# Kernel optimization log

Hardware: AMD Instinct MI355X
Metric: run time of the kernel (lower is better)

Reference implementation:

```python
import jax, jax.numpy as jnp
import numpy as np

B, S, DM, H, NM, PRED = 32, 512, 512, 8, 4, 96
DK = DM // H
C1 = (NM + 7) // 2  # 5
C2 = (NM + 7) // 4  # 2
FC_IN = C2 * (S // 2)  # 512
EPS_NORM = 1e-12
EPS_LN = 1e-5


def _pos_encoding(seq_len, d):
    pos = np.arange(seq_len, dtype=np.float32)[:, None]
    div = np.exp(np.arange(0, d, 2, dtype=np.float32) * (-np.log(10000.0) / d))
    pe = np.zeros((seq_len, d), np.float32)
    pe[:, 0::2] = np.sin(pos * div)
    pe[:, 1::2] = np.cos(pos * div)
    return jnp.asarray(pe)

PE = _pos_encoding(S, DM)


def setup_inputs() -> dict:
    key = jax.random.key(0)
    ks = jax.random.split(key, 24)
    g = lambda k, shape, s: (jax.random.normal(k, shape, dtype=jnp.float32) * s)
    inp = {
        "x": g(ks[0], (B, S, 7), 1.0),
        "emb_W": g(ks[1], (4, DM), 0.5),
        "emb_b": jnp.zeros((DM,), jnp.float32),
        "Wq": g(ks[2], (NM, DM, DM), DM ** -0.5),
        "bq": jnp.zeros((NM, DM), jnp.float32),
        "Wk": g(ks[3], (NM, DM, DM), DM ** -0.5),
        "bk": jnp.zeros((NM, DM), jnp.float32),
        "Wv": g(ks[4], (NM, DM, DM), DM ** -0.5),
        "bv": jnp.zeros((NM, DM), jnp.float32),
        "Wo": g(ks[5], (NM, DM, DM), DM ** -0.5),
        "bo": jnp.zeros((NM, DM), jnp.float32),
        "conv1_w": g(ks[6], (C1, NM * DM, 3), (NM * DM * 3) ** -0.5),
        "conv1_b": jnp.zeros((C1,), jnp.float32),
        "conv2_w": g(ks[7], (C2, C1, 3), (C1 * 3) ** -0.5),
        "conv2_b": jnp.zeros((C2,), jnp.float32),
        "fc1_w": g(ks[8], (FC_IN, 256), FC_IN ** -0.5),
        "fc1_b": jnp.zeros((256,), jnp.float32),
        "fc2_w": g(ks[9], (256, 128), 256 ** -0.5),
        "fc2_b": jnp.zeros((128,), jnp.float32),
        "fc3_w": g(ks[10], (128, PRED), 128 ** -0.5),
        "fc3_b": jnp.zeros((PRED,), jnp.float32),
        "ln_g": jnp.ones((PRED,), jnp.float32),
        "ln_b": jnp.zeros((PRED,), jnp.float32),
    }
    return inp


def _l2norm(v):
    n = jnp.linalg.norm(v, axis=-1, keepdims=True)
    return v / jnp.maximum(n, EPS_NORM)


def reference(x, emb_W, emb_b, Wq, bq, Wk, bk, Wv, bv, Wo, bo,
              conv1_w, conv1_b, conv2_w, conv2_b,
              fc1_w, fc1_b, fc2_w, fc2_b, fc3_w, fc3_b, ln_g, ln_b):
    b, s, _ = x.shape
    static = x[:, :, :3]                     # [B,S,3]
    dynamic = x[:, :, 3:]                    # [B,S,4]
    # per-modality input: [dynamic_i | static] -> [B,M,S,4]
    mod_in = jnp.concatenate([
        dynamic.transpose(0, 2, 1)[..., None],
        jnp.broadcast_to(static[:, None], (b, NM, s, 3)),
    ], axis=-1)
    h = jnp.einsum('bmsf,fd->bmsd', mod_in, emb_W) + emb_b  # shared embedding
    h = h + PE[None, None, :s, :]

    # per-modality multi-head cosine attention (stacked over modality axis m)
    def proj(W, bias):
        y = jnp.einsum('bmsd,mde->bmse', h, W) + bias[None, :, None, :]
        return y.reshape(b, NM, s, H, DK).transpose(0, 1, 3, 2, 4)  # [B,M,H,S,DK]

    Q = _l2norm(proj(Wq, bq))
    K = _l2norm(proj(Wk, bk))
    V = proj(Wv, bv)
    scores = jnp.einsum('bmhsk,bmhtk->bmhst', Q, K)
    attn = jax.nn.softmax(scores, axis=-1)
    ctx = jnp.einsum('bmhst,bmhtk->bmhsk', attn, V)
    ctx = ctx.transpose(0, 1, 3, 2, 4).reshape(b, NM, s, DM)
    out = jnp.einsum('bmsd,mde->bmse', ctx, Wo) + bo[None, :, None, :]

    # concat modalities along feature dim: [B,S,M*DM]
    combined = out.transpose(0, 2, 1, 3).reshape(b, s, NM * DM)

    # conv stack (NCW layout), kernel 3, padding 1
    c = combined.transpose(0, 2, 1)  # [B, M*DM, S]
    dn = ('NCH', 'OIH', 'NCH')
    c = jax.lax.conv_general_dilated(c, conv1_w, (1,), ((1, 1),), dimension_numbers=dn) + conv1_b[None, :, None]
    c = jax.nn.elu(c)
    c = jax.lax.conv_general_dilated(c, conv2_w, (1,), ((1, 1),), dimension_numbers=dn) + conv2_b[None, :, None]
    c = jax.nn.elu(c)
    # max pool k=2 stride=2
    c = c.reshape(b, C2, s // 2, 2).max(axis=-1)
    flat = c.reshape(b, -1)  # [B, FC_IN]

    z = jax.nn.elu(flat @ fc1_w + fc1_b)
    z = jax.nn.elu(z @ fc2_w + fc2_b)
    z = z @ fc3_w + fc3_b  # [B, PRED]

    mu = jnp.mean(z, axis=-1, keepdims=True)
    var = jnp.var(z, axis=-1, keepdims=True)
    z = (z - mu) / jnp.sqrt(var + EPS_LN) * ln_g + ln_b
    return z.reshape(b, PRED, 1)
```

## Files before the change

### kernel.cpp

```cpp
#include <hip/hip_runtime.h>
#include <math.h>

typedef unsigned short u16;
typedef unsigned int u32;
typedef __attribute__((ext_vector_type(8))) short short8;
typedef __attribute__((ext_vector_type(4))) float f32x4;
typedef __attribute__((ext_vector_type(16))) float f32x16;
typedef __attribute__((ext_vector_type(4))) u32 u32x4;
typedef __attribute__((ext_vector_type(2))) u32 u32x2;

__device__ inline u16 f2b(float f) {
  u32 u = __builtin_bit_cast(u32, f);
  u32 r = u + 0x7fffu + ((u >> 16) & 1u);
  return (u16)(r >> 16);
}
__device__ inline float b2f(u16 b) {
  return __builtin_bit_cast(float, (u32)b << 16);
}
__device__ inline u32 cvtpk(float lo, float hi) {
  u32 r;
  asm("v_cvt_pk_bf16_f32 %0, %1, %2" : "=v"(r) : "v"(lo), "v"(hi));
  return r;
}
__device__ inline float eluf(float x) { return x > 0.f ? x : expf(x) - 1.f; }

__device__ inline f32x4 mfma16(short8 a, short8 b, f32x4 c) {
  return __builtin_amdgcn_mfma_f32_16x16x32_bf16(a, b, c, 0, 0, 0);
}
__device__ inline f32x16 mfma32(short8 a, short8 b, f32x16 c) {
  return __builtin_amdgcn_mfma_f32_32x32x16_bf16(a, b, c, 0, 0, 0);
}
__device__ inline void gload16(const u16* g, u16* l) {
  __builtin_amdgcn_global_load_lds((__attribute__((address_space(1))) void*)(g),
                                   (__attribute__((address_space(3))) void*)(l),
                                   16, 0, 0);
}

__global__ __launch_bounds__(256) void prep_misc(
    const float* __restrict__ emb_b, const float* __restrict__ bq,
    const float* __restrict__ bk, const float* __restrict__ bv,
    const float* __restrict__ Wq, const float* __restrict__ Wk,
    const float* __restrict__ Wv, const float* __restrict__ embW,
    const float* __restrict__ Wo, const float* __restrict__ bo,
    const float* __restrict__ w1, u16* __restrict__ A_pe,
    float* __restrict__ pb_bias, float* __restrict__ EW,
    u16* __restrict__ WEFFT, float* __restrict__ bias_t,
    u16* __restrict__ WTqkv) {
  __shared__ float smem[64 * 65];
  const int bid = blockIdx.x, t = threadIdx.x;
  if (bid < 512) {
    int s = bid;
    float div = expf((2.f * t) * (-9.210340371976184f / 512.f));
    float arg = (float)s * div;
    A_pe[s * 512 + 2 * t] = f2b(sinf(arg) + emb_b[2 * t]);
    A_pe[s * 512 + 2 * t + 1] = f2b(cosf(arg) + emb_b[2 * t + 1]);
  } else if (bid < 536) {
    int i = (bid - 512) * 256 + t;
    int z = i >> 9, e = i & 511;
    int ty = z >> 2, m = z & 3;
    const float* bp = (ty == 0) ? bq : (ty == 1) ? bk : bv;
    pb_bias[i] = bp[m * 512 + e];
  } else if (bid < 584) {
    int idx = bid - 536;
    int z = idx >> 2, ch = idx & 3;
    const float* W =
        ((z < 4) ? Wq : (z < 8) ? Wk : Wv) + (long)(z & 3) * 262144;
    int el = t & 127, dh = t >> 7;
    int e = ch * 128 + el;
    float a[4] = {};
    for (int d = dh * 256; d < dh * 256 + 256; ++d) {
      float wv = W[(long)d * 512 + e];
#pragma unroll
      for (int f = 0; f < 4; ++f) a[f] += embW[f * 512 + d] * wv;
    }
#pragma unroll
    for (int f = 0; f < 4; ++f) smem[(dh * 4 + f) * 128 + el] = a[f];
    __syncthreads();
    if (t < 128) {
#pragma unroll
      for (int f = 0; f < 4; ++f)
        EW[((long)z * 4 + f) * 512 + e] =
            smem[f * 128 + el] + smem[(4 + f) * 128 + el];
    }
  } else if (bid < 1097) {
    const int wb = bid - 584;
    const int w = t >> 6, l = t & 63;
    if (wb < 512) {
      int idx = wb * 4 + w;
      int m = idx >> 9, d = idx & 511;
      const float* wrow = Wo + ((long)m * 512 + d) * 512;
      float a[15] = {};
#pragma unroll
      for (int i = 0; i < 8; ++i) {
        int e = l * 8 + i;
        float wv = wrow[e];
#pragma unroll
        for (int o = 0; o < 5; ++o)
#pragma unroll
          for (int k = 0; k < 3; ++k)
            a[o * 3 + k] += wv * w1[((long)o * 2048 + m * 512 + e) * 3 + k];
      }
#pragma unroll
      for (int j = 0; j < 15; ++j) {
        float v = a[j];
        for (int o = 1; o < 64; o <<= 1) v += __shfl_xor(v, o);
        if (l == 0) WEFFT[((long)m * 16 + j) * 512 + d] = f2b(v);
      }
      if (l == 0) WEFFT[((long)m * 16 + 15) * 512 + d] = 0;
    } else if (w == 0) {
      float a[15] = {};
      for (int c = l; c < 2048; c += 64) {
        float bv = bo[c];
#pragma unroll
        for (int o = 0; o < 5; ++o)
#pragma unroll
          for (int k = 0; k < 3; ++k)
            a[o * 3 + k] += bv * w1[((long)o * 2048 + c) * 3 + k];
      }
#pragma unroll
      for (int j = 0; j < 15; ++j) {
        float v = a[j];
        for (int o = 1; o < 64; o <<= 1) v += __shfl_xor(v, o);
        if (l == 0) bias_t[j] = v;
      }
      if (l == 0) bias_t[15] = 0.f;
    }
  } else {
    int bidt = bid - 1097;
    int mid = bidt >> 6, rest = bidt & 63;
    int d0 = (rest >> 3) * 64, e0 = (rest & 7) * 64;
    const float* W =
        ((mid < 4) ? Wq : (mid < 8) ? Wk : Wv) + (long)(mid & 3) * 262144;
    u16* WT = WTqkv + (long)mid * 262144;
    float(*tile)[65] = (float(*)[65])smem;
    int dr = t >> 2, ec = (t & 3) * 16;
#pragma unroll
    for (int j = 0; j < 16; j += 4) {
      float4 v = *(const float4*)&W[(long)(d0 + dr) * 512 + e0 + ec + j];
      tile[dr][ec + j] = v.x;
      tile[dr][ec + j + 1] = v.y;
      tile[dr][ec + j + 2] = v.z;
      tile[dr][ec + j + 3] = v.w;
    }
    __syncthreads();
    int er = t >> 2, dc = (t & 3) * 16;
    u16 tmp[16] __attribute__((aligned(16)));
#pragma unroll
    for (int j = 0; j < 16; ++j) tmp[j] = f2b(tile[dc + j][er]);
    *(short8*)&WT[(long)(e0 + er) * 512 + d0 + dc] = *(short8*)&tmp[0];
    *(short8*)&WT[(long)(e0 + er) * 512 + d0 + dc + 8] = *(short8*)&tmp[8];
  }
}

template <bool OBF>
__global__ __launch_bounds__(256) void gemm_bt(
    const u16* __restrict__ A, long sAz, int lda, const u16* __restrict__ BT,
    const float* __restrict__ bias, void* __restrict__ out, long sOz, int ldo) {
  __shared__ u16 As[3][128 * 32];
  __shared__ u16 Bs[3][128 * 32];
  const int z = blockIdx.z;
  const int tid = threadIdx.x, w = tid >> 6, l = tid & 63;
  const long row0 = (long)blockIdx.y * 128;
  const u16* Ab = A + (long)z * sAz + row0 * lda;
  const u16* Bb = BT + (long)z * 262144 + (long)blockIdx.x * 128 * 512;
  const u16* ga = Ab + (long)(w * 32 + (l >> 2)) * lda + (l & 3) * 8;
  const u16* gb = Bb + (long)(w * 32 + (l >> 2)) * 512 + (l & 3) * 8;
  f32x4 acc[4][4] = {};
  const int wr = (w >> 1) * 64, wc = (w & 1) * 64;

#define GSTAGE(BF, KT)                                                        \
  {                                                                           \
    gload16(ga + (KT)*32, &As[BF][w * 32 * 32]);                              \
    gload16(ga + (KT)*32 + 16 * lda, &As[BF][w * 32 * 32 + 16 * 32]);         \
    gload16(gb + (KT)*32, &Bs[BF][w * 32 * 32]);                              \
    gload16(gb + (KT)*32 + 16 * 512, &Bs[BF][w * 32 * 32 + 16 * 32]);         \
  }

#define GTILE(KT, CUR, NXT)                                                   \
  {                                                                           \
    if ((KT) < 15) {                                                          \
      GSTAGE(NXT, (KT) + 1);                                                  \
      asm volatile("s_waitcnt vmcnt(4)" ::: "memory");                        \
    } else {                                                                  \
      asm volatile("s_waitcnt vmcnt(0)" ::: "memory");                        \
    }                                                                         \
    __builtin_amdgcn_s_barrier();                                             \
    __builtin_amdgcn_sched_barrier(0);                                        \
    short8 af[4], bf[4];                                                      \
    _Pragma("unroll") for (int i = 0; i < 4; ++i) af[i] =                     \
        *(const short8*)&As[CUR][(wr + i * 16 + (l & 15)) * 32 +              \
                                 (l >> 4) * 8];                               \
    _Pragma("unroll") for (int i = 0; i < 4; ++i) bf[i] =                     \
        *(const short8*)&Bs[CUR][(wc + i * 16 + (l & 15)) * 32 +              \
                                 (l >> 4) * 8];                               \
    _Pragma("unroll") for (int i = 0; i < 4; ++i) _Pragma("unroll")           \
        for (int j = 0; j < 4; ++j) acc[i][j] =                               \
            mfma16(af[i], bf[j], acc[i][j]);                                  \
    __builtin_amdgcn_sched_barrier(0);                                        \
  }

  GSTAGE(0, 0);
  GTILE(0, 0, 1);  GTILE(1, 1, 2);  GTILE(2, 2, 0);  GTILE(3, 0, 1);
  GTILE(4, 1, 2);  GTILE(5, 2, 0);  GTILE(6, 0, 1);  GTILE(7, 1, 2);
  GTILE(8, 2, 0);  GTILE(9, 0, 1);  GTILE(10, 1, 2); GTILE(11, 2, 0);
  GTILE(12, 0, 1); GTILE(13, 1, 2); GTILE(14, 2, 0); GTILE(15, 0, 1);
#undef GTILE
#undef GSTAGE

  const int colB = blockIdx.x * 128 + wc;
#pragma unroll
  for (int i = 0; i < 4; ++i)
#pragma unroll
    for (int j = 0; j < 4; ++j) {
      int col = colB + j * 16 + (l & 15);
      float bb = bias[(long)z * 512 + col];
#pragma unroll
      for (int q = 0; q < 4; ++q) {
        long r = row0 + wr + i * 16 + (l >> 4) * 4 + q;
        float v = acc[i][j][q] + bb;
        if (OBF)
          ((u16*)out)[(long)z * sOz + r * ldo + col] = f2b(v);
        else
          ((float*)out)[(long)z * sOz + r * ldo + col] = v;
      }
    }
}

__global__ __launch_bounds__(256) void qkv_fused(
    const float* __restrict__ x, const float* __restrict__ EW,
    const u16* __restrict__ PB, u16* __restrict__ Q, u16* __restrict__ K,
    u16* __restrict__ VT, long mstride) {
  __shared__ float ews[3][4][64];
  __shared__ u16 vtile[64][72];
  const int bh = blockIdx.x;
  const int st = blockIdx.y;
  const int m = blockIdx.z;
  const int b = bh >> 3, h = bh & 7;
  const int hoff = h * 64;
  const int t = threadIdx.x;
  if (t < 192) {
    int ty = t >> 6, dk = t & 63;
#pragma unroll
    for (int f = 0; f < 4; ++f)
      ews[ty][f][dk] = EW[(((long)(ty * 4 + m)) * 4 + f) * 512 + hoff + dk];
  }
  __syncthreads();
  const int sr = t >> 2, cq = t & 3;
  const int s = st * 64 + sr;
  const long rid = (long)b * 512 + s;
  const float* xr = x + rid * 7;
  const float xd = xr[3 + m], x0 = xr[0], x1 = xr[1], x2 = xr[2];
  const long obase = (long)m * mstride + rid * 512 + hoff + cq * 16;

  float res[3][16];
#pragma unroll
  for (int ty = 0; ty < 3; ++ty) {
    const u16* pbp =
        PB + (((long)(ty * 4 + m)) * 512 + s) * 512 + hoff + cq * 16;
    short8 pbv0 = *(const short8*)pbp;
    short8 pbv1 = *(const short8*)(pbp + 8);
#pragma unroll
    for (int j = 0; j < 16; ++j) {
      int dk = cq * 16 + j;
      u16 pb = (u16)(j < 8 ? pbv0[j] : pbv1[j - 8]);
      res[ty][j] = xd * ews[ty][0][dk] + x0 * ews[ty][1][dk] +
                   x1 * ews[ty][2][dk] + x2 * ews[ty][3][dk] + b2f(pb);
    }
  }
#pragma unroll
  for (int ty = 0; ty < 2; ++ty) {
    float ss = 0.f;
#pragma unroll
    for (int j = 0; j < 16; ++j) ss += res[ty][j] * res[ty][j];
    ss += __shfl_xor(ss, 1);
    ss += __shfl_xor(ss, 2);
    float sc = 1.f / fmaxf(sqrtf(ss), 1e-12f);
    u32 o[8];
#pragma unroll
    for (int jj = 0; jj < 8; ++jj)
      o[jj] = cvtpk(res[ty][2 * jj] * sc, res[ty][2 * jj + 1] * sc);
    u16* P = ty ? K : Q;
    *(u32x4*)&P[obase] = *(u32x4*)&o[0];
    *(u32x4*)&P[obase + 8] = *(u32x4*)&o[4];
  }
  {
    u32 o[8];
#pragma unroll
    for (int jj = 0; jj < 8; ++jj)
      o[jj] = cvtpk(res[2][2 * jj], res[2][2 * jj + 1]);
    *(short8*)&vtile[sr][cq * 16] = *(short8*)&o[0];
    *(short8*)&vtile[sr][cq * 16 + 8] = *(short8*)&o[4];
  }
  __syncthreads();
  {
    int kr = t >> 2, sc2 = (t & 3) * 16;
    u16 tmp[16] __attribute__((aligned(16)));
#pragma unroll
    for (int j = 0; j < 16; ++j) tmp[j] = vtile[sc2 + j][kr];
    long gdst = (long)m * mstride + ((long)bh * 64 + kr) * 512 + st * 64 + sc2;
    *(short8*)&VT[gdst] = *(short8*)&tmp[0];
    *(short8*)&VT[gdst + 8] = *(short8*)&tmp[8];
  }
}

__global__ __launch_bounds__(512, 2) void attn_kernel(
    const u16* Qg, const u16* __restrict__ Kg, const u16* __restrict__ VTg,
    u16* ctxg, long mstride) {
  __shared__ u16 Kb[4][64][64];
  __shared__ u16 Vb[4][64][64];
  const int wgid = (blockIdx.x & 7) * 256 + (blockIdx.x >> 3);
  const int qp = wgid & 1;
  const int mz = wgid >> 1;
  const int m = mz & 3;
  const int bh = mz >> 2;
  const u16* Q = Qg + (long)m * mstride;
  const u16* K = Kg + (long)m * mstride;
  const u16* VT = VTg + (long)m * mstride;
  u16* ctx = ctxg + (long)m * mstride;
  const int b = bh >> 3, h = bh & 7;
  const int tid = threadIdx.x, w = tid >> 6, l = tid & 63;
  const int lq = l & 31, hi = l >> 5, l7 = l & 7;
  const long rowbase = (long)b * 512;
  const int hoff = h * 64;
  const int rw = l >> 3, gch = (l & 7) ^ rw;
  const int qrow = qp * 256 + w * 32;

  short8 qf[4];
  {
    const u16* qrp = Q + (rowbase + qrow + lq) * 512 + hoff + hi * 8;
#pragma unroll
    for (int dc = 0; dc < 4; ++dc) qf[dc] = *(const short8*)(qrp + dc * 16);
  }

  short8 ones;
#pragma unroll
  for (int i = 0; i < 8; ++i) ones[i] = (short)0x3F80;

  f32x16 o_acc[2] = {};
  f32x16 l_acc = {};

  const u16* Kgbase = K + rowbase * 512 + hoff + gch * 8;
  const u16* Vgbase = VT + (long)bh * 64 * 512 + gch * 8;

#define STAGE(bf, kt)                                                         \
  {                                                                           \
    int rr = w * 8;                                                           \
    gload16(Kgbase + (long)((kt)*64 + rr + rw) * 512, &Kb[bf][rr][0]);        \
    gload16(Vgbase + (long)(rr + rw) * 512 + (kt)*64, &Vb[bf][rr][0]);        \
  }

#define TILE(KT, CUR, NXT)                                                    \
  {                                                                           \
    if ((KT) < 6) {                                                           \
      STAGE(NXT, (KT) + 2);                                                   \
      asm volatile("s_waitcnt vmcnt(4)" ::: "memory");                        \
    } else if ((KT) == 6) {                                                   \
      asm volatile("s_waitcnt vmcnt(2)" ::: "memory");                        \
    } else {                                                                  \
      asm volatile("s_waitcnt vmcnt(0)" ::: "memory");                        \
    }                                                                         \
    __builtin_amdgcn_s_barrier();                                             \
    __builtin_amdgcn_sched_barrier(0);                                        \
    __builtin_amdgcn_s_setprio(1);                                            \
    _Pragma("unroll") for (int ktile = 0; ktile < 2; ++ktile) {               \
      f32x16 s = {};                                                          \
      _Pragma("unroll") for (int dc = 0; dc < 4; ++dc) {                      \
        short8 kf = *(const short8*)((const char*)&Kb[CUR][ktile * 32 + lq]   \
                                         [0] +                                \
                                     (((dc * 2 + hi) ^ l7) * 16));            \
        s = mfma32(kf, qf[dc], s);                                            \
      }                                                                       \
      float p[16];                                                            \
      _Pragma("unroll") for (int r = 0; r < 16; ++r) p[r] = __expf(s[r]);     \
      u32 s0a = cvtpk(p[0], p[1]), s0b = cvtpk(p[4], p[5]);                   \
      u32 s1a = cvtpk(p[2], p[3]), s1b = cvtpk(p[6], p[7]);                   \
      u32 s2a = cvtpk(p[8], p[9]), s2b = cvtpk(p[12], p[13]);                 \
      u32 s3a = cvtpk(p[10], p[11]), s3b = cvtpk(p[14], p[15]);               \
      asm("v_permlane32_swap_b32 %0, %1" : "+v"(s0a), "+v"(s0b));             \
      asm("v_permlane32_swap_b32 %0, %1" : "+v"(s1a), "+v"(s1b));             \
      asm("v_permlane32_swap_b32 %0, %1" : "+v"(s2a), "+v"(s2b));             \
      asm("v_permlane32_swap_b32 %0, %1" : "+v"(s3a), "+v"(s3b));             \
      u32x4 f0v = {s0a, s1a, s0b, s1b};                                       \
      u32x4 f1v = {s2a, s3a, s2b, s3b};                                       \
      short8 bf0 = __builtin_bit_cast(short8, f0v);                           \
      short8 bf1 = __builtin_bit_cast(short8, f1v);                           \
      _Pragma("unroll") for (int kk2 = 0; kk2 < 2; ++kk2) {                   \
        const int kc = ktile * 2 + kk2;                                       \
        short8 pb = kk2 ? bf1 : bf0;                                          \
        l_acc = mfma32(ones, pb, l_acc);                                      \
        _Pragma("unroll") for (int dt = 0; dt < 2; ++dt) {                    \
          short8 vf =                                                         \
              *(const short8*)((const char*)&Vb[CUR][dt * 32 + lq][0] +       \
                               (((kc * 2 + hi) ^ l7) * 16));                  \
          o_acc[dt] = mfma32(vf, pb, o_acc[dt]);                              \
        }                                                                     \
      }                                                                       \
    }                                                                         \
    __builtin_amdgcn_s_setprio(0);                                            \
    __builtin_amdgcn_sched_barrier(0);                                        \
  }

  STAGE(0, 0);
  STAGE(1, 1);
  TILE(0, 0, 2);
  TILE(1, 1, 3);
  TILE(2, 2, 0);
  TILE(3, 3, 1);
  TILE(4, 0, 2);
  TILE(5, 1, 3);
  TILE(6, 2, 0);
  TILE(7, 3, 1);
#undef TILE
#undef STAGE
  const float inv = 1.f / l_acc[0];
  u16* crow = ctx + (rowbase + qrow + lq) * 512 + hoff + hi * 4;
#pragma unroll
  for (int dt = 0; dt < 2; ++dt)
#pragma unroll
    for (int rq = 0; rq < 4; ++rq) {
      u32 w0 = cvtpk(o_acc[dt][rq * 4 + 0] * inv, o_acc[dt][rq * 4 + 1] * inv);
      u32 w1 = cvtpk(o_acc[dt][rq * 4 + 2] * inv, o_acc[dt][rq * 4 + 3] * inv);
      u32x2 pr = {w0, w1};
      *(u32x2*)&crow[dt * 32 + rq * 8] = pr;
    }
}

__global__ __launch_bounds__(64) void t_gemm(const u16* __restrict__ ctx4,
                                             const u16* __restrict__ WEFFT,
                                             float* __restrict__ t) {
  const int l = threadIdx.x;
  const long r0 = (long)blockIdx.x * 16;
  f32x4 acc = {};
#pragma unroll
  for (int m = 0; m < 4; ++m) {
    const u16* A =
        ctx4 + (long)m * 8388608 + (r0 + (l & 15)) * 512 + (l >> 4) * 8;
    const u16* Bb = WEFFT + m * 8192 + (l & 15) * 512 + (l >> 4) * 8;
#pragma unroll
    for (int kt = 0; kt < 16; ++kt) {
      short8 af = *(const short8*)(A + kt * 32);
      short8 bf = *(const short8*)(Bb + kt * 32);
      acc = mfma16(af, bf, acc);
    }
  }
#pragma unroll
  for (int q = 0; q < 4; ++q)
    t[(r0 + (l >> 4) * 4 + q) * 16 + (l & 15)] = acc[q];
}

__global__ __launch_bounds__(512) void tail_fused(
    const float* __restrict__ t, const float* __restrict__ bias_t,
    const float* __restrict__ b1, const float* __restrict__ w2,
    const float* __restrict__ b2, const float* __restrict__ fw1,
    const float* __restrict__ fb1, const float* __restrict__ fw2,
    const float* __restrict__ fb2, const float* __restrict__ fw3,
    const float* __restrict__ fb3, const float* __restrict__ g,
    const float* __restrict__ be, float* __restrict__ out) {
  __shared__ float ts[512][16];
  __shared__ float c1s[5][512];
  __shared__ float flat[512];
  __shared__ float z1p[2][256];
  __shared__ float z1[256];
  __shared__ float z2p[2][128];
  __shared__ float z2[128];
  __shared__ float z3[96];
  int b = blockIdx.x, tid = threadIdx.x;
  const float4* tsrc = (const float4*)(t + (long)b * 8192);
  float4* tdst = (float4*)&ts[0][0];
#pragma unroll
  for (int i = 0; i < 4; ++i) tdst[tid + i * 512] = tsrc[tid + i * 512];
  __syncthreads();
#pragma unroll
  for (int i = 0; i < 5; ++i) {
    int idx = tid + i * 512;
    int o = idx >> 9, s = idx & 511;
    float a = b1[o];
#pragma unroll
    for (int k = 0; k < 3; ++k) {
      int ss = s + k - 1;
      if (ss >= 0 && ss < 512) a += ts[ss][o * 3 + k] + bias_t[o * 3 + k];
    }
    c1s[o][s] = eluf(a);
  }
  __syncthreads();
  {
    int r = tid;
    int o = r >> 8, sp = r & 255;
    float mx = -1e30f;
#pragma unroll
    for (int sd = 0; sd < 2; ++sd) {
      int s = sp * 2 + sd;
      float a = b2[o];
#pragma unroll
      for (int ic = 0; ic < 5; ++ic)
#pragma unroll
        for (int k = 0; k < 3; ++k) {
          int ss = s + k - 1;
          if (ss >= 0 && ss < 512) a += c1s[ic][ss] * w2[(o * 5 + ic) * 3 + k];
        }
      mx = fmaxf(mx, eluf(a));
    }
    flat[r] = mx;
  }
  __syncthreads();
  {
    int o = tid & 255, part = tid >> 8;
    float a = 0.f;
    const float* wp = fw1 + (long)part * 256 * 256 + o;
    const float* xp = flat + part * 256;
#pragma unroll 8
    for (int i = 0; i < 256; ++i) a += xp[i] * wp[i * 256];
    z1p[part][o] = a;
  }
  __syncthreads();
  if (tid < 256) z1[tid] = eluf(fb1[tid] + z1p[0][tid] + z1p[1][tid]);
  __syncthreads();
  if (tid < 256) {
    int o = tid & 127, part = tid >> 7;
    float a = 0.f;
    const float* wp = fw2 + (long)part * 128 * 128 + o;
    const float* xp = z1 + part * 128;
#pragma unroll 8
    for (int i = 0; i < 128; ++i) a += xp[i] * wp[i * 128];
    z2p[part][o] = a;
  }
  __syncthreads();
  if (tid < 128) z2[tid] = eluf(fb2[tid] + z2p[0][tid] + z2p[1][tid]);
  __syncthreads();
  if (tid < 96) {
    float a = fb3[tid];
#pragma unroll 8
    for (int i = 0; i < 128; ++i) a += z2[i] * fw3[i * 96 + tid];
    z3[tid] = a;
  }
  __syncthreads();
  if (tid < 96) {
    float mu = 0.f;
    for (int j = 0; j < 96; ++j) mu += z3[j];
    mu *= (1.f / 96.f);
    float sq = 0.f;
    for (int j = 0; j < 96; ++j) {
      float d = z3[j] - mu;
      sq += d * d;
    }
    float var = sq * (1.f / 96.f);
    out[b * 96 + tid] = (z3[tid] - mu) / sqrtf(var + 1e-5f) * g[tid] + be[tid];
  }
}

extern "C" void kernel_launch(void* const* d_in, const int* in_sizes, int n_in,
                              void* d_out, int out_size, void* d_ws,
                              size_t ws_size, hipStream_t stream) {
  (void)in_sizes; (void)n_in; (void)out_size;
  const float* x    = (const float*)d_in[0];
  const float* embW = (const float*)d_in[1];
  const float* embB = (const float*)d_in[2];
  const float* Wq   = (const float*)d_in[3];
  const float* bq   = (const float*)d_in[4];
  const float* Wk   = (const float*)d_in[5];
  const float* bk   = (const float*)d_in[6];
  const float* Wv   = (const float*)d_in[7];
  const float* bv   = (const float*)d_in[8];
  const float* Wo   = (const float*)d_in[9];
  const float* bo   = (const float*)d_in[10];
  const float* c1w  = (const float*)d_in[11];
  const float* c1b  = (const float*)d_in[12];
  const float* c2w  = (const float*)d_in[13];
  const float* c2b  = (const float*)d_in[14];
  const float* f1w  = (const float*)d_in[15];
  const float* f1b  = (const float*)d_in[16];
  const float* f2w  = (const float*)d_in[17];
  const float* f2b_ = (const float*)d_in[18];
  const float* f3w  = (const float*)d_in[19];
  const float* f3b  = (const float*)d_in[20];
  const float* lng  = (const float*)d_in[21];
  const float* lnb  = (const float*)d_in[22];
  float* out = (float*)d_out;

  char* p = (char*)d_ws;
  const size_t NEED = 215736384;
  if (ws_size < NEED) return;
  const long MS = 8388608;

  u16*   A_pe    = (u16*)(p + 0);
  u16*   WTqkv   = (u16*)(p + 524288);
  float* pb_bias = (float*)(p + 6815744);
  float* EW      = (float*)(p + 6840320);
  u16*   PB      = (u16*)(p + 6938624);
  u16*   Q4      = (u16*)(p + 13230080);
  u16*   K4      = (u16*)(p + 80338944);
  u16*   VT4     = (u16*)(p + 147447808);
  u16*   ctx4    = Q4;
  u16*   WEFFT   = (u16*)(p + 214556672);
  float* bias_t  = (float*)(p + 214622208);
  float* t_buf   = (float*)(p + 214622272);

  prep_misc<<<1865, 256, 0, stream>>>(embB, bq, bk, bv, Wq, Wk, Wv, embW, Wo,
                                      bo, c1w, A_pe, pb_bias, EW, WEFFT,
                                      bias_t, WTqkv);
  gemm_bt<true><<<dim3(4, 4, 12), 256, 0, stream>>>(
      A_pe, 0, 512, WTqkv, pb_bias, (void*)PB, 262144, 512);

  qkv_fused<<<dim3(256, 8, 4), 256, 0, stream>>>(x, EW, PB, Q4, K4, VT4, MS);
  attn_kernel<<<2048, 512, 0, stream>>>(Q4, K4, VT4, ctx4, MS);

  t_gemm<<<1024, 64, 0, stream>>>(ctx4, WEFFT, t_buf);
  tail_fused<<<32, 512, 0, stream>>>(t_buf, bias_t, c1b, c2w, c2b, f1w, f1b,
                                     f2w, f2b_, f3w, f3b, lng, lnb, out);
}
```

Measured before the change: 224.8 us.

## Compute normalized Q inside attention kernel instead of materializing it

The Q projection and L2 normalization move out of the QKV prep kernel and into the attention kernel prologue. Each wave rebuilds its Q fragments from x, the effective embedding weights and the positional-bias buffer, so the 64 MB bf16 Q tensor is no longer written and read back. The prep kernel now produces only K and the transposed V. Positional-encoding setup also switches to fast __expf/__sinf/__cosf intrinsics, which slightly lowers accuracy for large arguments.

New measurement: 222.5 us. About the same (-1.0%).

```diff
diff --git a/kernel.cpp b/kernel.cpp
--- a/kernel.cpp
+++ b/kernel.cpp
@@ -50,10 +50,10 @@
   const int bid = blockIdx.x, t = threadIdx.x;
   if (bid < 512) {
     int s = bid;
-    float div = expf((2.f * t) * (-9.210340371976184f / 512.f));
+    float div = __expf((2.f * t) * (-9.210340371976184f / 512.f));
     float arg = (float)s * div;
-    A_pe[s * 512 + 2 * t] = f2b(sinf(arg) + emb_b[2 * t]);
-    A_pe[s * 512 + 2 * t + 1] = f2b(cosf(arg) + emb_b[2 * t + 1]);
+    A_pe[s * 512 + 2 * t] = f2b(__sinf(arg) + emb_b[2 * t]);
+    A_pe[s * 512 + 2 * t + 1] = f2b(__cosf(arg) + emb_b[2 * t + 1]);
   } else if (bid < 536) {
     int i = (bid - 512) * 256 + t;
     int z = i >> 9, e = i & 511;
@@ -226,11 +226,11 @@
     }
 }
 
-__global__ __launch_bounds__(256) void qkv_fused(
+__global__ __launch_bounds__(256) void kv_fused(
     const float* __restrict__ x, const float* __restrict__ EW,
-    const u16* __restrict__ PB, u16* __restrict__ Q, u16* __restrict__ K,
-    u16* __restrict__ VT, long mstride) {
-  __shared__ float ews[3][4][64];
+    const u16* __restrict__ PB, u16* __restrict__ K, u16* __restrict__ VT,
+    long mstride) {
+  __shared__ float ews[2][4][64];
   __shared__ u16 vtile[64][72];
   const int bh = blockIdx.x;
   const int st = blockIdx.y;
@@ -238,11 +238,12 @@
   const int b = bh >> 3, h = bh & 7;
   const int hoff = h * 64;
   const int t = threadIdx.x;
-  if (t < 192) {
-    int ty = t >> 6, dk = t & 63;
+  if (t < 128) {
+    int ir = t >> 6, dk = t & 63;
+    int z = (ir + 1) * 4 + m;
 #pragma unroll
     for (int f = 0; f < 4; ++f)
-      ews[ty][f][dk] = EW[(((long)(ty * 4 + m)) * 4 + f) * 512 + hoff + dk];
+      ews[ir][f][dk] = EW[((long)z * 4 + f) * 512 + hoff + dk];
   }
   __syncthreads();
   const int sr = t >> 2, cq = t & 3;
@@ -252,42 +253,40 @@
   const float xd = xr[3 + m], x0 = xr[0], x1 = xr[1], x2 = xr[2];
   const long obase = (long)m * mstride + rid * 512 + hoff + cq * 16;
 
-  float res[3][16];
-#pragma unroll
-  for (int ty = 0; ty < 3; ++ty) {
-    const u16* pbp =
-        PB + (((long)(ty * 4 + m)) * 512 + s) * 512 + hoff + cq * 16;
+  float res[2][16];
+#pragma unroll
+  for (int ir = 0; ir < 2; ++ir) {
+    int z = (ir + 1) * 4 + m;
+    const u16* pbp = PB + (((long)z * 512 + s)) * 512 + hoff + cq * 16;
     short8 pbv0 = *(const short8*)pbp;
     short8 pbv1 = *(const short8*)(pbp + 8);
 #pragma unroll
     for (int j = 0; j < 16; ++j) {
       int dk = cq * 16 + j;
       u16 pb = (u16)(j < 8 ? pbv0[j] : pbv1[j - 8]);
-      res[ty][j] = xd * ews[ty][0][dk] + x0 * ews[ty][1][dk] +
-                   x1 * ews[ty][2][dk] + x2 * ews[ty][3][dk] + b2f(pb);
-    }
-  }
-#pragma unroll
-  for (int ty = 0; ty < 2; ++ty) {
+      res[ir][j] = xd * ews[ir][0][dk] + x0 * ews[ir][1][dk] +
+                   x1 * ews[ir][2][dk] + x2 * ews[ir][3][dk] + b2f(pb);
+    }
+  }
+  {
     float ss = 0.f;
 #pragma unroll
-    for (int j = 0; j < 16; ++j) ss += res[ty][j] * res[ty][j];
+    for (int j = 0; j < 16; ++j) ss += res[0][j] * res[0][j];
     ss += __shfl_xor(ss, 1);
     ss += __shfl_xor(ss, 2);
     float sc = 1.f / fmaxf(sqrtf(ss), 1e-12f);
     u32 o[8];
 #pragma unroll
     for (int jj = 0; jj < 8; ++jj)
-      o[jj] = cvtpk(res[ty][2 * jj] * sc, res[ty][2 * jj + 1] * sc);
-    u16* P = ty ? K : Q;
-    *(u32x4*)&P[obase] = *(u32x4*)&o[0];
-    *(u32x4*)&P[obase + 8] = *(u32x4*)&o[4];
+      o[jj] = cvtpk(res[0][2 * jj] * sc, res[0][2 * jj + 1] * sc);
+    *(u32x4*)&K[obase] = *(u32x4*)&o[0];
+    *(u32x4*)&K[obase + 8] = *(u32x4*)&o[4];
   }
   {
     u32 o[8];
 #pragma unroll
     for (int jj = 0; jj < 8; ++jj)
-      o[jj] = cvtpk(res[2][2 * jj], res[2][2 * jj + 1]);
+      o[jj] = cvtpk(res[1][2 * jj], res[1][2 * jj + 1]);
     *(short8*)&vtile[sr][cq * 16] = *(short8*)&o[0];
     *(short8*)&vtile[sr][cq * 16 + 8] = *(short8*)&o[4];
   }
@@ -304,16 +303,17 @@
 }
 
 __global__ __launch_bounds__(512, 2) void attn_kernel(
-    const u16* Qg, const u16* __restrict__ Kg, const u16* __restrict__ VTg,
-    u16* ctxg, long mstride) {
+    const float* __restrict__ x, const float* __restrict__ EW,
+    const u16* __restrict__ PB, const u16* __restrict__ Kg,
+    const u16* __restrict__ VTg, u16* __restrict__ ctxg, long mstride) {
   __shared__ u16 Kb[4][64][64];
   __shared__ u16 Vb[4][64][64];
+  __shared__ float ewsq[4][64];
   const int wgid = (blockIdx.x & 7) * 256 + (blockIdx.x >> 3);
   const int qp = wgid & 1;
   const int mz = wgid >> 1;
   const int m = mz & 3;
   const int bh = mz >> 2;
-  const u16* Q = Qg + (long)m * mstride;
   const u16* K = Kg + (long)m * mstride;
   const u16* VT = VTg + (long)m * mstride;
   u16* ctx = ctxg + (long)m * mstride;
@@ -325,11 +325,43 @@
   const int rw = l >> 3, gch = (l & 7) ^ rw;
   const int qrow = qp * 256 + w * 32;
 
+  if (tid < 256) {
+    int f = tid >> 6, dk = tid & 63;
+    ewsq[f][dk] = EW[((long)m * 4 + f) * 512 + hoff + dk];
+  }
+  __syncthreads();
+
   short8 qf[4];
   {
-    const u16* qrp = Q + (rowbase + qrow + lq) * 512 + hoff + hi * 8;
-#pragma unroll
-    for (int dc = 0; dc < 4; ++dc) qf[dc] = *(const short8*)(qrp + dc * 16);
+    const int s_q = qrow + lq;
+    const float* xr = x + (rowbase + s_q) * 7;
+    const float xd = xr[3 + m], x0 = xr[0], x1 = xr[1], x2 = xr[2];
+    float qv[4][8];
+    float ss = 0.f;
+#pragma unroll
+    for (int dc = 0; dc < 4; ++dc) {
+      const int dk0 = dc * 16 + hi * 8;
+      const u16* pbq = PB + ((long)m * 512 + s_q) * 512 + hoff + dk0;
+      short8 pbv = *(const short8*)pbq;
+#pragma unroll
+      for (int j = 0; j < 8; ++j) {
+        int dk = dk0 + j;
+        float v = xd * ewsq[0][dk] + x0 * ewsq[1][dk] + x1 * ewsq[2][dk] +
+                  x2 * ewsq[3][dk] + b2f((u16)pbv[j]);
+        qv[dc][j] = v;
+        ss += v * v;
+      }
+    }
+    ss += __shfl_xor(ss, 32);
+    float sc = 1.f / fmaxf(sqrtf(ss), 1e-12f);
+#pragma unroll
+    for (int dc = 0; dc < 4; ++dc) {
+      u32x4 pk = {cvtpk(qv[dc][0] * sc, qv[dc][1] * sc),
+                  cvtpk(qv[dc][2] * sc, qv[dc][3] * sc),
+                  cvtpk(qv[dc][4] * sc, qv[dc][5] * sc),
+                  cvtpk(qv[dc][6] * sc, qv[dc][7] * sc)};
+      qf[dc] = __builtin_bit_cast(short8, pk);
+    }
   }
 
   short8 ones;
@@ -587,10 +619,9 @@
   float* pb_bias = (float*)(p + 6815744);
   float* EW      = (float*)(p + 6840320);
   u16*   PB      = (u16*)(p + 6938624);
-  u16*   Q4      = (u16*)(p + 13230080);
+  u16*   ctx4    = (u16*)(p + 13230080);
   u16*   K4      = (u16*)(p + 80338944);
   u16*   VT4     = (u16*)(p + 147447808);
-  u16*   ctx4    = Q4;
   u16*   WEFFT   = (u16*)(p + 214556672);
   float* bias_t  = (float*)(p + 214622208);
   float* t_buf   = (float*)(p + 214622272);
@@ -601,8 +632,8 @@
   gemm_bt<true><<<dim3(4, 4, 12), 256, 0, stream>>>(
       A_pe, 0, 512, WTqkv, pb_bias, (void*)PB, 262144, 512);
 
-  qkv_fused<<<dim3(256, 8, 4), 256, 0, stream>>>(x, EW, PB, Q4, K4, VT4, MS);
-  attn_kernel<<<2048, 512, 0, stream>>>(Q4, K4, VT4, ctx4, MS);
+  kv_fused<<<dim3(256, 8, 4), 256, 0, stream>>>(x, EW, PB, K4, VT4, MS);
+  attn_kernel<<<2048, 512, 0, stream>>>(x, EW, PB, K4, VT4, ctx4, MS);
 
   t_gemm<<<1024, 64, 0, stream>>>(ctx4, WEFFT, t_buf);
   tail_fused<<<32, 512, 0, stream>>>(t_buf, bias_t, c1b, c2w, c2b, f1w, f1b,
```
